# Kernel tuning notes

Hardware: AMD Instinct MI355X
Metric: run time of the kernel (lower is better)

The kernel has to match this reference:

```python
import jax, jax.numpy as jnp
import numpy as np

# anchor encoding indices: [x,y,z,log w,log l,log h,sin,cos,vx,vy,vz]
NUM_HEADS = 8
LN_EPS = 1e-5


def layer_norm(x, g, b):
    mu = jnp.mean(x, axis=-1, keepdims=True)
    var = jnp.var(x, axis=-1, keepdims=True)
    return (x - mu) * jax.lax.rsqrt(var + LN_EPS) * g + b


def align_anchors_to_frame(anchor, Tm):
    # anchor: (..., N, 11), Tm: (..., 4, 4)
    R = Tm[..., :3, :3]
    t = Tm[..., :3, 3]
    center = jnp.einsum('...ij,...nj->...ni', R, anchor[..., 0:3]) + t[..., None, :]
    size = anchor[..., 3:6]
    yaw = jnp.einsum('...ij,...nj->...ni', R[..., :2, :2], anchor[..., 6:8])
    vel = jnp.einsum('...ij,...nj->...ni', R, anchor[..., 8:11])
    return jnp.concatenate([center, size, yaw, vel], axis=-1)


def setup_inputs() -> dict:
    key = jax.random.key(0)
    ks = jax.random.split(key, 12)
    B, T, N, C, E, A = 2, 12, 1024, 256, 256, 11
    inp = {
        'seq_features': jax.random.normal(ks[0], (B, T, N, C), jnp.float32),
        'seq_anchors': jax.random.normal(ks[1], (B, T, N, A), jnp.float32),
        'T_ego_his2cur': jax.random.normal(ks[2], (B, T, 4, 4), jnp.float32),
        'Wf': jax.random.normal(ks[3], (E, C), jnp.float32) * (C ** -0.5),
        'bf': jnp.zeros((E,), jnp.float32),
        'Wa': jax.random.normal(ks[4], (E, A), jnp.float32) * (A ** -0.5),
        'ba': jnp.zeros((E,), jnp.float32),
        'Win': jax.random.normal(ks[5], (3 * E, E), jnp.float32) * (E ** -0.5),
        'bin_': jnp.zeros((3 * E,), jnp.float32),
        'gamma': jnp.ones((E,), jnp.float32),
        'beta': jnp.zeros((E,), jnp.float32),
    }
    return inp


def reference(seq_features, seq_anchors, T_ego_his2cur, Wf, bf, Wa, ba, Win, bin_, gamma, beta):
    B, T, N, C = seq_features.shape
    E = gamma.shape[0]
    H = NUM_HEADS
    D = E // H

    feat_cur = seq_features[:, 1:]    # (B,T-1,N,C)
    feat_prev = seq_features[:, :-1]
    anc_cur = seq_anchors[:, 1:]
    anc_prev = align_anchors_to_frame(seq_anchors[:, :-1], T_ego_his2cur[:, 1:])

    tok_cur = layer_norm(feat_cur @ Wf.T + bf + anc_cur @ Wa.T + ba, gamma, beta)
    tok_prev = layer_norm(feat_prev @ Wf.T + bf + anc_prev @ Wa.T + ba, gamma, beta)

    Wq, Wk = Win[:E], Win[E:2 * E]
    bq, bk = bin_[:E], bin_[E:2 * E]
    scale = np.float32(D) ** np.float32(-0.5)
    q = ((tok_cur @ Wq.T + bq) * scale).reshape(B, T - 1, N, H, D)
    k = (tok_prev @ Wk.T + bk).reshape(B, T - 1, N, H, D)

    scores = jnp.einsum('btnhd,btmhd->bthnm', q, k)  # (B,T-1,H,N,N)
    attn = jax.nn.softmax(scores, axis=-1).mean(axis=2)  # head-averaged weights

    eye = jnp.broadcast_to(jnp.eye(N, dtype=seq_features.dtype), (B, 1, N, N))
    return jnp.concatenate([eye, attn], axis=1)  # (B,T,N,N)
```

## Files before the change

kernel.cpp:

```cpp
#include <hip/hip_runtime.h>
#include <hip/hip_bf16.h>
#include <math.h>

#define LN_EPS 1e-5f

typedef short bf16x8 __attribute__((ext_vector_type(8)));
typedef float f32x4 __attribute__((ext_vector_type(4)));

__device__ inline short f2bf(float f) {
  union { float f; unsigned u; } v; v.f = f;
  unsigned r = v.u + 0x7FFFu + ((v.u >> 16) & 1u);
  return (short)(r >> 16);
}
__device__ inline float bf2f(unsigned short s) {
  union { unsigned u; float f; } v; v.u = ((unsigned)s) << 16;
  return v.f;
}
__device__ inline float fast_exp2(float x) {
#if __has_builtin(__builtin_amdgcn_exp2f)
  return __builtin_amdgcn_exp2f(x);
#else
  return __expf(x * 0.69314718056f);
#endif
}

__global__ __launch_bounds__(256) void convert_kernel(const float* __restrict__ Wf,
    const float* __restrict__ Win, short* __restrict__ Wfb, short* __restrict__ Wqkb)
{
  size_t i = ((size_t)blockIdx.x * 256 + threadIdx.x) * 8;
  const float* src;
  short* dst;
  if (i < 65536) { src = Wf + i; dst = Wfb + i; }
  else { src = Win + (i - 65536); dst = Wqkb + (i - 65536); }
  f32x4 x0 = *(const f32x4*)src;
  f32x4 x1 = *(const f32x4*)(src + 4);
  bf16x8 v;
  v[0] = f2bf(x0[0]); v[1] = f2bf(x0[1]); v[2] = f2bf(x0[2]); v[3] = f2bf(x0[3]);
  v[4] = f2bf(x1[0]); v[5] = f2bf(x1[1]); v[6] = f2bf(x1[2]); v[7] = f2bf(x1[3]);
  *(bf16x8*)dst = v;
}

__global__ __launch_bounds__(256, 2) void feat_ln(const float* __restrict__ Af,
    const short* __restrict__ Wb, const float* __restrict__ bfv,
    const float* __restrict__ anchors, const float* __restrict__ Tego,
    const float* __restrict__ Wa, const float* __restrict__ ba,
    const float* __restrict__ gamma, const float* __restrict__ beta,
    short* __restrict__ tok_cur, short* __restrict__ tok_prev)
{
  const int which = blockIdx.y;
  const int row0 = blockIdx.x * 64;
  const int s24 = row0 >> 10;
  const int b = s24 / 12, t = s24 - b * 12;
  if (which == 0 && t == 0) return;
  if (which == 1 && t == 11) return;

  __shared__ short ldb[256][40];
  __shared__ float ldWaT[11][256];
  __shared__ float aST[11][64];
  const int tid = threadIdx.x;
  const int wid = tid >> 6, lane = tid & 63;
  const int quad = lane >> 4, l15 = lane & 15;
  const int n0 = row0 & 1023;
  const int srow = tid >> 2, sseg = tid & 3;

  {
    float wv[11];
    #pragma unroll
    for (int jj = 0; jj < 11; ++jj) wv[jj] = Wa[(size_t)tid * 11 + jj];
    #pragma unroll
    for (int jj = 0; jj < 11; ++jj) ldWaT[jj][tid] = wv[jj];
  }
  if (tid < 64) {
    const float* ap = anchors + ((size_t)s24 * 1024 + n0 + tid) * 11;
    float a[11];
    #pragma unroll
    for (int j = 0; j < 11; ++j) a[j] = ap[j];
    if (which == 1) {
      const float* Tm = Tego + ((size_t)b * 12 + t + 1) * 16;
      float r00 = Tm[0], r01 = Tm[1], r02 = Tm[2],  t0 = Tm[3];
      float r10 = Tm[4], r11 = Tm[5], r12 = Tm[6],  t1 = Tm[7];
      float r20 = Tm[8], r21 = Tm[9], r22 = Tm[10], t2 = Tm[11];
      float a0 = a[0], a1 = a[1], a2 = a[2];
      float a6 = a[6], a7 = a[7], a8 = a[8], a9 = a[9], a10 = a[10];
      a[0] = r00 * a0 + r01 * a1 + r02 * a2 + t0;
      a[1] = r10 * a0 + r11 * a1 + r12 * a2 + t1;
      a[2] = r20 * a0 + r21 * a1 + r22 * a2 + t2;
      a[6] = r00 * a6 + r01 * a7;
      a[7] = r10 * a6 + r11 * a7;
      a[8] = r00 * a8 + r01 * a9 + r02 * a10;
      a[9] = r10 * a8 + r11 * a9 + r12 * a10;
      a[10] = r20 * a8 + r21 * a9 + r22 * a10;
    }
    #pragma unroll
    for (int j = 0; j < 11; ++j) aST[j][tid] = a[j];
  }

  f32x4 z = {0.f, 0.f, 0.f, 0.f};
  f32x4 acc[16];
  #pragma unroll
  for (int j = 0; j < 16; ++j) acc[j] = z;

  const float* arp = Af + (size_t)(row0 + wid * 16 + l15) * 256 + quad * 8;
  const short* wgp = Wb + (size_t)srow * 256 + sseg * 8;

  f32x4 xa0 = *(const f32x4*)(arp);
  f32x4 xa1 = *(const f32x4*)(arp + 4);

  #pragma unroll 1
  for (int ks = 0; ks < 8; ++ks) {
    const int kk = ks * 32;
    bf16x8 w0 = *(const bf16x8*)(wgp + kk);
    bf16x8 w1 = *(const bf16x8*)(wgp + 64 * 256 + kk);
    bf16x8 w2 = *(const bf16x8*)(wgp + 128 * 256 + kk);
    bf16x8 w3 = *(const bf16x8*)(wgp + 192 * 256 + kk);
    bf16x8 af;
    af[0] = f2bf(xa0[0]); af[1] = f2bf(xa0[1]); af[2] = f2bf(xa0[2]); af[3] = f2bf(xa0[3]);
    af[4] = f2bf(xa1[0]); af[5] = f2bf(xa1[1]); af[6] = f2bf(xa1[2]); af[7] = f2bf(xa1[3]);
    if (ks < 7) {
      xa0 = *(const f32x4*)(arp + kk + 32);
      xa1 = *(const f32x4*)(arp + kk + 36);
    }
    *(bf16x8*)&ldb[srow][sseg * 8]       = w0;
    *(bf16x8*)&ldb[srow + 64][sseg * 8]  = w1;
    *(bf16x8*)&ldb[srow + 128][sseg * 8] = w2;
    *(bf16x8*)&ldb[srow + 192][sseg * 8] = w3;
    __syncthreads();
    #pragma unroll
    for (int j = 0; j < 16; ++j) {
      bf16x8 bq = *(const bf16x8*)&ldb[j * 16 + l15][quad * 8];
      acc[j] = __builtin_amdgcn_mfma_f32_16x16x32_bf16(af, bq, acc[j], 0, 0, 0);
    }
    __syncthreads();
  }

  const int rbase = wid * 16 + quad * 4;
  #pragma unroll
  for (int jj = 0; jj < 11; ++jj) {
    f32x4 av = *(const f32x4*)&aST[jj][rbase];
    #pragma unroll
    for (int j = 0; j < 16; ++j) {
      float wv = ldWaT[jj][j * 16 + l15];
      #pragma unroll
      for (int r = 0; r < 4; ++r) acc[j][r] += wv * av[r];
    }
  }

  float s1[4] = {0.f, 0.f, 0.f, 0.f};
  float s2[4] = {0.f, 0.f, 0.f, 0.f};
  #pragma unroll
  for (int j = 0; j < 16; ++j) {
    const int col = j * 16 + l15;
    const float cb = bfv[col] + ba[col];
    #pragma unroll
    for (int r = 0; r < 4; ++r) {
      float v = acc[j][r] + cb;
      acc[j][r] = v;
      s1[r] += v; s2[r] += v * v;
    }
  }
  #pragma unroll
  for (int r = 0; r < 4; ++r) {
    #pragma unroll
    for (int off = 1; off < 16; off <<= 1) {
      s1[r] += __shfl_xor(s1[r], off);
      s2[r] += __shfl_xor(s2[r], off);
    }
  }
  float mean[4], rstd[4];
  #pragma unroll
  for (int r = 0; r < 4; ++r) {
    mean[r] = s1[r] * (1.0f / 256.0f);
    float var = s2[r] * (1.0f / 256.0f) - mean[r] * mean[r];
    rstd[r] = rsqrtf(var + LN_EPS);
  }

  short* dst = which ? tok_prev : tok_cur;
  const size_t tokbase = which ? (size_t)(b * 11 + t) * 1024
                               : (size_t)(b * 11 + t - 1) * 1024;
  #pragma unroll
  for (int j = 0; j < 16; ++j) {
    const int col = j * 16 + l15;
    const float g = gamma[col], be = beta[col];
    #pragma unroll
    for (int r = 0; r < 4; ++r) {
      const int n = n0 + wid * 16 + quad * 4 + r;
      dst[(tokbase + n) * 256 + col] = f2bf((acc[j][r] - mean[r]) * rstd[r] * g + be);
    }
  }
}

__global__ __launch_bounds__(256) void gemm_qk(const short* __restrict__ tokc,
    const short* __restrict__ tokp, const short* __restrict__ Wqkb,
    const float* __restrict__ binv, short* __restrict__ qb, short* __restrict__ kb)
{
  const int sel = blockIdx.z;
  const short* Ap = sel ? tokp : tokc;
  const short* W = Wqkb + (size_t)sel * 65536;
  const float* bias = binv + sel * 256;
  const float alpha = sel ? 1.0f : 0.17677669529663687f * 1.4426950408889634f;
  short* Out = sel ? kb : qb;

  __shared__ short lda[128][40];
  __shared__ short ldb[128][40];
  const int tid = threadIdx.x;
  const int bm = blockIdx.x * 128, bn = blockIdx.y * 128;
  const int wid = tid >> 6, lane = tid & 63;
  const int quad = lane >> 4, l15 = lane & 15;
  const int wm = (wid & 1) * 64, wn = (wid >> 1) * 64;
  const int srow = tid >> 2, sseg = tid & 3;

  f32x4 z = {0.f, 0.f, 0.f, 0.f};
  f32x4 acc[4][4];
  #pragma unroll
  for (int i = 0; i < 4; ++i)
    #pragma unroll
    for (int j = 0; j < 4; ++j) acc[i][j] = z;

  const short* a0 = Ap + (size_t)(bm + srow) * 256 + sseg * 8;
  const short* a1 = Ap + (size_t)(bm + srow + 64) * 256 + sseg * 8;
  const short* b0 = W + (size_t)(bn + srow) * 256 + sseg * 8;
  const short* b1 = W + (size_t)(bn + srow + 64) * 256 + sseg * 8;

  for (int kk = 0; kk < 256; kk += 32) {
    *(bf16x8*)&lda[srow][sseg * 8]      = *(const bf16x8*)(a0 + kk);
    *(bf16x8*)&lda[srow + 64][sseg * 8] = *(const bf16x8*)(a1 + kk);
    *(bf16x8*)&ldb[srow][sseg * 8]      = *(const bf16x8*)(b0 + kk);
    *(bf16x8*)&ldb[srow + 64][sseg * 8] = *(const bf16x8*)(b1 + kk);
    __syncthreads();
    bf16x8 af[4], bq[4];
    #pragma unroll
    for (int i = 0; i < 4; ++i) {
      af[i] = *(const bf16x8*)&lda[wm + i * 16 + l15][quad * 8];
      bq[i] = *(const bf16x8*)&ldb[wn + i * 16 + l15][quad * 8];
    }
    #pragma unroll
    for (int i = 0; i < 4; ++i)
      #pragma unroll
      for (int j = 0; j < 4; ++j)
        acc[i][j] = __builtin_amdgcn_mfma_f32_16x16x32_bf16(af[i], bq[j], acc[i][j], 0, 0, 0);
    __syncthreads();
  }

  #pragma unroll
  for (int i = 0; i < 4; ++i)
    #pragma unroll
    for (int j = 0; j < 4; ++j)
      #pragma unroll
      for (int r = 0; r < 4; ++r) {
        int grow = bm + wm + i * 16 + quad * 4 + r;
        int gcol = bn + wn + j * 16 + l15;
        float v = (acc[i][j][r] + bias[gcol]) * alpha;
        int btr = grow >> 10, nn = grow & 1023, h = gcol >> 5, d = gcol & 31;
        Out[(((size_t)btr * 8 + h) * 1024 + nn) * 32 + d] = f2bf(v);
      }
}

__global__ __launch_bounds__(256) void denom_kernel(const short* __restrict__ q,
  const short* __restrict__ k, float* __restrict__ dinv)
{
  __shared__ short kst[2][4096];
  const int tid = threadIdx.x, wid = tid >> 6, lane = tid & 63;
  const int quad = lane >> 4, l15 = lane & 15;
  const int h = blockIdx.y, bt = blockIdx.z;
  const int n0 = blockIdx.x * 128 + wid * 32;
  const size_t base = ((size_t)bt * 8 + h) * 32768;
  bf16x8 qf0 = *(const bf16x8*)(q + base + (size_t)(n0 + l15) * 32 + quad * 8);
  bf16x8 qf1 = *(const bf16x8*)(q + base + (size_t)(n0 + 16 + l15) * 32 + quad * 8);
  const short* ksA = k + base + (size_t)(wid * 16) * 32 + lane * 8;
  const short* ksB = k + base + (size_t)((wid + 4) * 16) * 32 + lane * 8;
  const int wswz = ((lane & 3) ^ ((lane >> 3) & 3)) * 8;
  const int rswz = (quad ^ ((l15 >> 1) & 3)) * 8;
  short* lwA = &kst[0][wid * 512 + (lane >> 2) * 32 + wswz];
  short* lwB = &kst[0][(wid + 4) * 512 + (lane >> 2) * 32 + wswz];

  f32x4 z = {0.f, 0.f, 0.f, 0.f};
  float s0 = 0.f, s1 = 0.f;

  bf16x8 stA = *(const bf16x8*)ksA;
  bf16x8 stB = *(const bf16x8*)ksB;
  *(bf16x8*)lwA = stA;
  *(bf16x8*)lwB = stB;
  __syncthreads();

  #pragma unroll 1
  for (int rd = 0; rd < 8; ++rd) {
    const int buf = rd & 1;
    if (rd < 7) {
      stA = *(const bf16x8*)(ksA + (size_t)(rd + 1) * 128 * 32);
      stB = *(const bf16x8*)(ksB + (size_t)(rd + 1) * 128 * 32);
    }
    #pragma unroll
    for (int s = 0; s < 8; ++s) {
      bf16x8 kf = *(const bf16x8*)&kst[buf][s * 512 + l15 * 32 + rswz];
      f32x4 c0 = __builtin_amdgcn_mfma_f32_16x16x32_bf16(kf, qf0, z, 0, 0, 0);
      f32x4 c1 = __builtin_amdgcn_mfma_f32_16x16x32_bf16(kf, qf1, z, 0, 0, 0);
      s0 += fast_exp2(c0[0]) + fast_exp2(c0[1]) + fast_exp2(c0[2]) + fast_exp2(c0[3]);
      s1 += fast_exp2(c1[0]) + fast_exp2(c1[1]) + fast_exp2(c1[2]) + fast_exp2(c1[3]);
    }
    if (rd < 7) {
      *(bf16x8*)(lwA + ((buf ^ 1) << 12)) = stA;
      *(bf16x8*)(lwB + ((buf ^ 1) << 12)) = stB;
    }
    __syncthreads();
  }
  s0 += __shfl_xor(s0, 16); s0 += __shfl_xor(s0, 32);
  s1 += __shfl_xor(s1, 16); s1 += __shfl_xor(s1, 32);
  if (quad == 0) {
    float* dp = dinv + ((size_t)bt * 8 + h) * 1024 + n0;
    dp[l15] = 1.f / s0;
    dp[16 + l15] = 1.f / s1;
  }
}

__global__ __launch_bounds__(256) void prob_kernel(const short* __restrict__ q,
  const short* __restrict__ k, const float* __restrict__ dinv, float* __restrict__ out)
{
  __shared__ short kst[2][4096];
  const int tid = threadIdx.x, wid = tid >> 6, lane = tid & 63;
  const int quad = lane >> 4, l15 = lane & 15;
  const int bt = blockIdx.z;
  const int n0 = blockIdx.x * 128 + wid * 32;
  const int mbase = blockIdx.y * 128;
  const int b = bt / 11, t = bt - b * 11;

  bf16x8 qf0[8], qf1[8];
  float invd0[8], invd1[8];
  #pragma unroll
  for (int h = 0; h < 8; ++h) {
    const size_t base = ((size_t)bt * 8 + h) * 32768;
    qf0[h] = *(const bf16x8*)(q + base + (size_t)(n0 + l15) * 32 + quad * 8);
    qf1[h] = *(const bf16x8*)(q + base + (size_t)(n0 + 16 + l15) * 32 + quad * 8);
    invd0[h] = dinv[((size_t)bt * 8 + h) * 1024 + n0 + l15] * 0.125f;
    invd1[h] = dinv[((size_t)bt * 8 + h) * 1024 + n0 + 16 + l15] * 0.125f;
  }
  const short* ksA = k + (((size_t)bt * 8 + wid    ) * 1024 + mbase) * 32 + lane * 8;
  const short* ksB = k + (((size_t)bt * 8 + wid + 4) * 1024 + mbase) * 32 + lane * 8;
  const int wswz = ((lane & 3) ^ ((lane >> 3) & 3)) * 8;
  const int rswz = (quad ^ ((l15 >> 1) & 3)) * 8;
  short* lwA = &kst[0][wid * 512 + (lane >> 2) * 32 + wswz];
  short* lwB = &kst[0][(wid + 4) * 512 + (lane >> 2) * 32 + wswz];

  float* ob0 = out + ((size_t)(b * 12 + t + 1) * 1024 + n0 + l15) * 1024
                   + mbase + quad * 4;
  float* ob1 = ob0 + (size_t)16 * 1024;
  f32x4 z = {0.f, 0.f, 0.f, 0.f};

  bf16x8 stA = *(const bf16x8*)ksA;
  bf16x8 stB = *(const bf16x8*)ksB;
  *(bf16x8*)lwA = stA;
  *(bf16x8*)lwB = stB;
  __syncthreads();

  #pragma unroll 1
  for (int mt = 0; mt < 8; ++mt) {
    const int buf = mt & 1;
    if (mt < 7) {
      stA = *(const bf16x8*)(ksA + (size_t)(mt + 1) * 16 * 32);
      stB = *(const bf16x8*)(ksB + (size_t)(mt + 1) * 16 * 32);
    }
    f32x4 P0 = z, P1 = z;
    #pragma unroll
    for (int h = 0; h < 8; ++h) {
      bf16x8 kf = *(const bf16x8*)&kst[buf][h * 512 + l15 * 32 + rswz];
      f32x4 c0 = __builtin_amdgcn_mfma_f32_16x16x32_bf16(kf, qf0[h], z, 0, 0, 0);
      f32x4 c1 = __builtin_amdgcn_mfma_f32_16x16x32_bf16(kf, qf1[h], z, 0, 0, 0);
      #pragma unroll
      for (int r = 0; r < 4; ++r) {
        P0[r] += fast_exp2(c0[r]) * invd0[h];
        P1[r] += fast_exp2(c1[r]) * invd1[h];
      }
    }
    *(f32x4*)(ob0 + mt * 16) = P0;
    *(f32x4*)(ob1 + mt * 16) = P1;
    if (mt < 7) {
      *(bf16x8*)(lwA + ((buf ^ 1) << 12)) = stA;
      *(bf16x8*)(lwB + ((buf ^ 1) << 12)) = stB;
    }
    __syncthreads();
  }
}

__global__ __launch_bounds__(256) void eye_kernel(float* __restrict__ out) {
  int gid = blockIdx.x * 256 + threadIdx.x;
  int b = gid >> 18, rem = gid & 262143;
  int n = rem >> 8, m4 = rem & 255;
  f32x4 v = {0.f, 0.f, 0.f, 0.f};
  int c = n - m4 * 4;
  if (c >= 0 && c < 4) v[c] = 1.0f;
  *(f32x4*)(out + (size_t)b * 12582912 + (size_t)n * 1024 + m4 * 4) = v;
}

extern "C" void kernel_launch(void* const* d_in, const int* in_sizes, int n_in,
                              void* d_out, int out_size, void* d_ws, size_t ws_size,
                              hipStream_t stream)
{
  const float* sf   = (const float*)d_in[0];
  const float* sa   = (const float*)d_in[1];
  const float* te   = (const float*)d_in[2];
  const float* Wf   = (const float*)d_in[3];
  const float* bfv  = (const float*)d_in[4];
  const float* Wa   = (const float*)d_in[5];
  const float* ba   = (const float*)d_in[6];
  const float* Win  = (const float*)d_in[7];
  const float* binv = (const float*)d_in[8];
  const float* gam  = (const float*)d_in[9];
  const float* bet  = (const float*)d_in[10];
  float* out = (float*)d_out;

  char* w = (char*)d_ws;
  short* tok_cur  = (short*)w;  w += 11534336;
  short* tok_prev = (short*)w;  w += 11534336;
  short* qb       = (short*)w;  w += 11534336;
  short* kb       = (short*)w;  w += 11534336;
  float* dinv     = (float*)w;  w += 720896;
  short* Wfb      = (short*)w;  w += 131072;
  short* Wqkb     = (short*)w;  w += 262144;

  convert_kernel<<<dim3(96), 256, 0, stream>>>(Wf, Win, Wfb, Wqkb);
  feat_ln<<<dim3(384, 2), 256, 0, stream>>>(sf, Wfb, bfv, sa, te, Wa, ba, gam, bet,
                                            tok_cur, tok_prev);
  gemm_qk<<<dim3(176, 2, 2), 256, 0, stream>>>(tok_cur, tok_prev, Wqkb, binv, qb, kb);
  denom_kernel<<<dim3(8, 8, 22), 256, 0, stream>>>(qb, kb, dinv);
  prob_kernel<<<dim3(8, 8, 22), 256, 0, stream>>>(qb, kb, dinv, out);
  eye_kernel<<<dim3(2048), 256, 0, stream>>>(out);
}
```

Baseline: 247.8 us.

## Share feature GEMM between cur/prev tokens and vectorize QK epilogue stores

feat_ln now runs once per 64-row feature block and reuses the feature projection for both the current-frame and previous-frame token outputs, applying separate anchor terms and LayerNorm for each. This halves the large fp32 feature reads and MFMA work in the token stage, at the cost of more registers from the second accumulator set and half as many blocks. Separately, gemm_qk swaps the MFMA operands so each lane holds four consecutive output columns, letting it write 4 bf16 values with a single short4 store and a vector bias load instead of scattered scalar stores.

New measurement: 245.2 us. Within noise of the previous version (-1.1%).

```diff
diff --git a/kernel.cpp b/kernel.cpp
--- a/kernel.cpp
+++ b/kernel.cpp
@@ -47,22 +47,22 @@
     const float* __restrict__ gamma, const float* __restrict__ beta,
     short* __restrict__ tok_cur, short* __restrict__ tok_prev)
 {
-  const int which = blockIdx.y;
   const int row0 = blockIdx.x * 64;
   const int s24 = row0 >> 10;
   const int b = s24 / 12, t = s24 - b * 12;
-  if (which == 0 && t == 0) return;
-  if (which == 1 && t == 11) return;
 
   __shared__ short ldb[256][40];
   __shared__ float ldWaT[11][256];
-  __shared__ float aST[11][64];
+  __shared__ float aSTc[11][64];
+  __shared__ float aSTp[11][64];
+  __shared__ float cbS[256];
   const int tid = threadIdx.x;
   const int wid = tid >> 6, lane = tid & 63;
   const int quad = lane >> 4, l15 = lane & 15;
   const int n0 = row0 & 1023;
   const int srow = tid >> 2, sseg = tid & 3;
 
+  cbS[tid] = bfv[tid] + ba[tid];
   {
     float wv[11];
     #pragma unroll
@@ -75,24 +75,26 @@
     float a[11];
     #pragma unroll
     for (int j = 0; j < 11; ++j) a[j] = ap[j];
-    if (which == 1) {
+    #pragma unroll
+    for (int j = 0; j < 11; ++j) aSTc[j][tid] = a[j];
+    if (t <= 10) {
       const float* Tm = Tego + ((size_t)b * 12 + t + 1) * 16;
       float r00 = Tm[0], r01 = Tm[1], r02 = Tm[2],  t0 = Tm[3];
       float r10 = Tm[4], r11 = Tm[5], r12 = Tm[6],  t1 = Tm[7];
       float r20 = Tm[8], r21 = Tm[9], r22 = Tm[10], t2 = Tm[11];
-      float a0 = a[0], a1 = a[1], a2 = a[2];
-      float a6 = a[6], a7 = a[7], a8 = a[8], a9 = a[9], a10 = a[10];
-      a[0] = r00 * a0 + r01 * a1 + r02 * a2 + t0;
-      a[1] = r10 * a0 + r11 * a1 + r12 * a2 + t1;
-      a[2] = r20 * a0 + r21 * a1 + r22 * a2 + t2;
-      a[6] = r00 * a6 + r01 * a7;
-      a[7] = r10 * a6 + r11 * a7;
-      a[8] = r00 * a8 + r01 * a9 + r02 * a10;
-      a[9] = r10 * a8 + r11 * a9 + r12 * a10;
-      a[10] = r20 * a8 + r21 * a9 + r22 * a10;
-    }
-    #pragma unroll
-    for (int j = 0; j < 11; ++j) aST[j][tid] = a[j];
+      float p0 = r00 * a[0] + r01 * a[1] + r02 * a[2] + t0;
+      float p1 = r10 * a[0] + r11 * a[1] + r12 * a[2] + t1;
+      float p2 = r20 * a[0] + r21 * a[1] + r22 * a[2] + t2;
+      float p6 = r00 * a[6] + r01 * a[7];
+      float p7 = r10 * a[6] + r11 * a[7];
+      float p8 = r00 * a[8] + r01 * a[9] + r02 * a[10];
+      float p9 = r10 * a[8] + r11 * a[9] + r12 * a[10];
+      float p10 = r20 * a[8] + r21 * a[9] + r22 * a[10];
+      aSTp[0][tid] = p0;  aSTp[1][tid] = p1;  aSTp[2][tid] = p2;
+      aSTp[3][tid] = a[3]; aSTp[4][tid] = a[4]; aSTp[5][tid] = a[5];
+      aSTp[6][tid] = p6;  aSTp[7][tid] = p7;
+      aSTp[8][tid] = p8;  aSTp[9][tid] = p9;  aSTp[10][tid] = p10;
+    }
   }
 
   f32x4 z = {0.f, 0.f, 0.f, 0.f};
@@ -134,59 +136,61 @@
   }
 
   const int rbase = wid * 16 + quad * 4;
-  #pragma unroll
-  for (int jj = 0; jj < 11; ++jj) {
-    f32x4 av = *(const f32x4*)&aST[jj][rbase];
+  auto emit = [&](const float (*aST)[64], short* dst, size_t tokbase) {
+    f32x4 d[16];
+    #pragma unroll
+    for (int j = 0; j < 16; ++j) d[j] = z;
+    #pragma unroll
+    for (int jj = 0; jj < 11; ++jj) {
+      f32x4 av = *(const f32x4*)&aST[jj][rbase];
+      #pragma unroll
+      for (int j = 0; j < 16; ++j) {
+        float wv = ldWaT[jj][j * 16 + l15];
+        #pragma unroll
+        for (int r = 0; r < 4; ++r) d[j][r] += wv * av[r];
+      }
+    }
+    float s1[4] = {0.f, 0.f, 0.f, 0.f};
+    float s2[4] = {0.f, 0.f, 0.f, 0.f};
     #pragma unroll
     for (int j = 0; j < 16; ++j) {
-      float wv = ldWaT[jj][j * 16 + l15];
-      #pragma unroll
-      for (int r = 0; r < 4; ++r) acc[j][r] += wv * av[r];
-    }
-  }
-
-  float s1[4] = {0.f, 0.f, 0.f, 0.f};
-  float s2[4] = {0.f, 0.f, 0.f, 0.f};
-  #pragma unroll
-  for (int j = 0; j < 16; ++j) {
-    const int col = j * 16 + l15;
-    const float cb = bfv[col] + ba[col];
+      const float cb = cbS[j * 16 + l15];
+      #pragma unroll
+      for (int r = 0; r < 4; ++r) {
+        float v = acc[j][r] + cb + d[j][r];
+        d[j][r] = v;
+        s1[r] += v; s2[r] += v * v;
+      }
+    }
     #pragma unroll
     for (int r = 0; r < 4; ++r) {
-      float v = acc[j][r] + cb;
-      acc[j][r] = v;
-      s1[r] += v; s2[r] += v * v;
-    }
-  }
-  #pragma unroll
-  for (int r = 0; r < 4; ++r) {
-    #pragma unroll
-    for (int off = 1; off < 16; off <<= 1) {
-      s1[r] += __shfl_xor(s1[r], off);
-      s2[r] += __shfl_xor(s2[r], off);
-    }
-  }
-  float mean[4], rstd[4];
-  #pragma unroll
-  for (int r = 0; r < 4; ++r) {
-    mean[r] = s1[r] * (1.0f / 256.0f);
-    float var = s2[r] * (1.0f / 256.0f) - mean[r] * mean[r];
-    rstd[r] = rsqrtf(var + LN_EPS);
-  }
-
-  short* dst = which ? tok_prev : tok_cur;
-  const size_t tokbase = which ? (size_t)(b * 11 + t) * 1024
-                               : (size_t)(b * 11 + t - 1) * 1024;
-  #pragma unroll
-  for (int j = 0; j < 16; ++j) {
-    const int col = j * 16 + l15;
-    const float g = gamma[col], be = beta[col];
+      #pragma unroll
+      for (int off = 1; off < 16; off <<= 1) {
+        s1[r] += __shfl_xor(s1[r], off);
+        s2[r] += __shfl_xor(s2[r], off);
+      }
+    }
+    float mean[4], rstd[4];
     #pragma unroll
     for (int r = 0; r < 4; ++r) {
-      const int n = n0 + wid * 16 + quad * 4 + r;
-      dst[(tokbase + n) * 256 + col] = f2bf((acc[j][r] - mean[r]) * rstd[r] * g + be);
-    }
-  }
+      mean[r] = s1[r] * (1.0f / 256.0f);
+      float var = s2[r] * (1.0f / 256.0f) - mean[r] * mean[r];
+      rstd[r] = rsqrtf(var + LN_EPS);
+    }
+    #pragma unroll
+    for (int j = 0; j < 16; ++j) {
+      const int col = j * 16 + l15;
+      const float g = gamma[col], be = beta[col];
+      #pragma unroll
+      for (int r = 0; r < 4; ++r) {
+        const int n = n0 + wid * 16 + quad * 4 + r;
+        dst[(tokbase + n) * 256 + col] = f2bf((d[j][r] - mean[r]) * rstd[r] * g + be);
+      }
+    }
+  };
+
+  if (t >= 1)  emit(aSTc, tok_cur,  (size_t)(b * 11 + t - 1) * 1024);
+  if (t <= 10) emit(aSTp, tok_prev, (size_t)(b * 11 + t) * 1024);
 }
 
 __global__ __launch_bounds__(256) void gemm_qk(const short* __restrict__ tokc,
@@ -237,22 +241,28 @@
     for (int i = 0; i < 4; ++i)
       #pragma unroll
       for (int j = 0; j < 4; ++j)
-        acc[i][j] = __builtin_amdgcn_mfma_f32_16x16x32_bf16(af[i], bq[j], acc[i][j], 0, 0, 0);
+        acc[i][j] = __builtin_amdgcn_mfma_f32_16x16x32_bf16(bq[j], af[i], acc[i][j], 0, 0, 0);
     __syncthreads();
   }
 
   #pragma unroll
-  for (int i = 0; i < 4; ++i)
-    #pragma unroll
-    for (int j = 0; j < 4; ++j)
-      #pragma unroll
-      for (int r = 0; r < 4; ++r) {
-        int grow = bm + wm + i * 16 + quad * 4 + r;
-        int gcol = bn + wn + j * 16 + l15;
-        float v = (acc[i][j][r] + bias[gcol]) * alpha;
-        int btr = grow >> 10, nn = grow & 1023, h = gcol >> 5, d = gcol & 31;
-        Out[(((size_t)btr * 8 + h) * 1024 + nn) * 32 + d] = f2bf(v);
-      }
+  for (int i = 0; i < 4; ++i) {
+    const int grow = bm + wm + i * 16 + l15;
+    const int btr = grow >> 10, nn = grow & 1023;
+    #pragma unroll
+    for (int j = 0; j < 4; ++j) {
+      const int gcol0 = bn + wn + j * 16;
+      const int h = gcol0 >> 5;
+      const int d0 = (gcol0 & 31) + quad * 4;
+      f32x4 bv = *(const f32x4*)(bias + gcol0 + quad * 4);
+      short4 o;
+      o.x = f2bf((acc[i][j][0] + bv[0]) * alpha);
+      o.y = f2bf((acc[i][j][1] + bv[1]) * alpha);
+      o.z = f2bf((acc[i][j][2] + bv[2]) * alpha);
+      o.w = f2bf((acc[i][j][3] + bv[3]) * alpha);
+      *(short4*)(Out + (((size_t)btr * 8 + h) * 1024 + nn) * 32 + d0) = o;
+    }
+  }
 }
 
 __global__ __launch_bounds__(256) void denom_kernel(const short* __restrict__ q,
@@ -417,8 +427,8 @@
   short* Wqkb     = (short*)w;  w += 262144;
 
   convert_kernel<<<dim3(96), 256, 0, stream>>>(Wf, Win, Wfb, Wqkb);
-  feat_ln<<<dim3(384, 2), 256, 0, stream>>>(sf, Wfb, bfv, sa, te, Wa, ba, gam, bet,
-                                            tok_cur, tok_prev);
+  feat_ln<<<dim3(384), 256, 0, stream>>>(sf, Wfb, bfv, sa, te, Wa, ba, gam, bet,
+                                         tok_cur, tok_prev);
   gemm_qk<<<dim3(176, 2, 2), 256, 0, stream>>>(tok_cur, tok_prev, Wqkb, binv, qb, kb);
   denom_kernel<<<dim3(8, 8, 22), 256, 0, stream>>>(qb, kb, dinv);
   prob_kernel<<<dim3(8, 8, 22), 256, 0, stream>>>(qb, kb, dinv, out);
```

## Fuse feature projection, layer norm and Q/K projection into one kernel

Applied to the files above, without the earlier changes.

Merges the feat_ln and gemm_qk kernels. Each block now computes the shared feature GEMM once for a 64-row tile and produces both the cur and prev token variants from it, since only the anchor term differs. It then layer-normalizes both, stages them in LDS as bf16, and projects them to Q and K directly with weights read from global memory. This removes the tok_cur/tok_prev round trip through global memory, one kernel launch, and the duplicated feature GEMM. In exchange it uses more LDS and registers per block, and the Q/K projection runs with only 384 blocks and unstaged weight loads.

Measured after the change: 269.4 us. 8.7% more time.

```diff
diff --git a/kernel.cpp b/kernel.cpp
--- a/kernel.cpp
+++ b/kernel.cpp
@@ -40,29 +40,35 @@
   *(bf16x8*)dst = v;
 }
 
-__global__ __launch_bounds__(256, 2) void feat_ln(const float* __restrict__ Af,
+__global__ __launch_bounds__(256, 2) void feat_qk(const float* __restrict__ Af,
     const short* __restrict__ Wb, const float* __restrict__ bfv,
     const float* __restrict__ anchors, const float* __restrict__ Tego,
     const float* __restrict__ Wa, const float* __restrict__ ba,
     const float* __restrict__ gamma, const float* __restrict__ beta,
-    short* __restrict__ tok_cur, short* __restrict__ tok_prev)
+    const short* __restrict__ Wqkb, const float* __restrict__ binv,
+    short* __restrict__ qb, short* __restrict__ kb)
 {
-  const int which = blockIdx.y;
   const int row0 = blockIdx.x * 64;
   const int s24 = row0 >> 10;
   const int b = s24 / 12, t = s24 - b * 12;
-  if (which == 0 && t == 0) return;
-  if (which == 1 && t == 11) return;
-
-  __shared__ short ldb[256][40];
-  __shared__ float ldWaT[11][256];
-  __shared__ float aST[11][64];
+  const bool do_cur = (t >= 1), do_prev = (t <= 10);
+
+  __shared__ __attribute__((aligned(16))) char smem[67584];
+  short (*ldb)[40]    = (short(*)[40])(smem);
+  float (*ldWaT)[256] = (float(*)[256])(smem + 20480);
+  float (*aSTc)[64]   = (float(*)[64])(smem + 31744);
+  float (*aSTp)[64]   = (float(*)[64])(smem + 34560);
+  float* cbS          = (float*)(smem + 37376);
+  short (*Acur)[264]  = (short(*)[264])(smem);
+  short (*Aprev)[264] = (short(*)[264])(smem + 33792);
+
   const int tid = threadIdx.x;
   const int wid = tid >> 6, lane = tid & 63;
   const int quad = lane >> 4, l15 = lane & 15;
   const int n0 = row0 & 1023;
   const int srow = tid >> 2, sseg = tid & 3;
 
+  cbS[tid] = bfv[tid] + ba[tid];
   {
     float wv[11];
     #pragma unroll
@@ -75,24 +81,23 @@
     float a[11];
     #pragma unroll
     for (int j = 0; j < 11; ++j) a[j] = ap[j];
-    if (which == 1) {
+    #pragma unroll
+    for (int j = 0; j < 11; ++j) aSTc[j][tid] = a[j];
+    if (do_prev) {
       const float* Tm = Tego + ((size_t)b * 12 + t + 1) * 16;
       float r00 = Tm[0], r01 = Tm[1], r02 = Tm[2],  t0 = Tm[3];
       float r10 = Tm[4], r11 = Tm[5], r12 = Tm[6],  t1 = Tm[7];
       float r20 = Tm[8], r21 = Tm[9], r22 = Tm[10], t2 = Tm[11];
-      float a0 = a[0], a1 = a[1], a2 = a[2];
-      float a6 = a[6], a7 = a[7], a8 = a[8], a9 = a[9], a10 = a[10];
-      a[0] = r00 * a0 + r01 * a1 + r02 * a2 + t0;
-      a[1] = r10 * a0 + r11 * a1 + r12 * a2 + t1;
-      a[2] = r20 * a0 + r21 * a1 + r22 * a2 + t2;
-      a[6] = r00 * a6 + r01 * a7;
-      a[7] = r10 * a6 + r11 * a7;
-      a[8] = r00 * a8 + r01 * a9 + r02 * a10;
-      a[9] = r10 * a8 + r11 * a9 + r12 * a10;
-      a[10] = r20 * a8 + r21 * a9 + r22 * a10;
-    }
-    #pragma unroll
-    for (int j = 0; j < 11; ++j) aST[j][tid] = a[j];
+      aSTp[0][tid] = r00 * a[0] + r01 * a[1] + r02 * a[2] + t0;
+      aSTp[1][tid] = r10 * a[0] + r11 * a[1] + r12 * a[2] + t1;
+      aSTp[2][tid] = r20 * a[0] + r21 * a[1] + r22 * a[2] + t2;
+      aSTp[3][tid] = a[3]; aSTp[4][tid] = a[4]; aSTp[5][tid] = a[5];
+      aSTp[6][tid] = r00 * a[6] + r01 * a[7];
+      aSTp[7][tid] = r10 * a[6] + r11 * a[7];
+      aSTp[8][tid] = r00 * a[8] + r01 * a[9] + r02 * a[10];
+      aSTp[9][tid] = r10 * a[8] + r11 * a[9] + r12 * a[10];
+      aSTp[10][tid] = r20 * a[8] + r21 * a[9] + r22 * a[10];
+    }
   }
 
   f32x4 z = {0.f, 0.f, 0.f, 0.f};
@@ -102,7 +107,6 @@
 
   const float* arp = Af + (size_t)(row0 + wid * 16 + l15) * 256 + quad * 8;
   const short* wgp = Wb + (size_t)srow * 256 + sseg * 8;
-
   f32x4 xa0 = *(const f32x4*)(arp);
   f32x4 xa1 = *(const f32x4*)(arp + 4);
 
@@ -134,125 +138,123 @@
   }
 
   const int rbase = wid * 16 + quad * 4;
+  f32x4 vcur[16], vprev[16];
+
+  #pragma unroll
+  for (int j = 0; j < 16; ++j) { vcur[j] = z; vprev[j] = z; }
   #pragma unroll
   for (int jj = 0; jj < 11; ++jj) {
-    f32x4 av = *(const f32x4*)&aST[jj][rbase];
+    f32x4 avc = *(const f32x4*)&aSTc[jj][rbase];
+    f32x4 avp = *(const f32x4*)&aSTp[jj][rbase];
     #pragma unroll
     for (int j = 0; j < 16; ++j) {
       float wv = ldWaT[jj][j * 16 + l15];
       #pragma unroll
-      for (int r = 0; r < 4; ++r) acc[j][r] += wv * av[r];
-    }
-  }
-
-  float s1[4] = {0.f, 0.f, 0.f, 0.f};
-  float s2[4] = {0.f, 0.f, 0.f, 0.f};
+      for (int r = 0; r < 4; ++r) {
+        vcur[j][r] += wv * avc[r];
+        vprev[j][r] += wv * avp[r];
+      }
+    }
+  }
+  float s1c[4] = {0,0,0,0}, s2c[4] = {0,0,0,0};
+  float s1p[4] = {0,0,0,0}, s2p[4] = {0,0,0,0};
   #pragma unroll
   for (int j = 0; j < 16; ++j) {
-    const int col = j * 16 + l15;
-    const float cb = bfv[col] + ba[col];
+    const float cb = cbS[j * 16 + l15];
     #pragma unroll
     for (int r = 0; r < 4; ++r) {
-      float v = acc[j][r] + cb;
-      acc[j][r] = v;
-      s1[r] += v; s2[r] += v * v;
+      float vc = acc[j][r] + cb + vcur[j][r];
+      float vp = acc[j][r] + cb + vprev[j][r];
+      vcur[j][r] = vc; vprev[j][r] = vp;
+      s1c[r] += vc; s2c[r] += vc * vc;
+      s1p[r] += vp; s2p[r] += vp * vp;
     }
   }
   #pragma unroll
   for (int r = 0; r < 4; ++r) {
     #pragma unroll
     for (int off = 1; off < 16; off <<= 1) {
-      s1[r] += __shfl_xor(s1[r], off);
-      s2[r] += __shfl_xor(s2[r], off);
-    }
-  }
-  float mean[4], rstd[4];
+      s1c[r] += __shfl_xor(s1c[r], off); s2c[r] += __shfl_xor(s2c[r], off);
+      s1p[r] += __shfl_xor(s1p[r], off); s2p[r] += __shfl_xor(s2p[r], off);
+    }
+  }
+  float mc[4], rc[4], mp[4], rp[4];
   #pragma unroll
   for (int r = 0; r < 4; ++r) {
-    mean[r] = s1[r] * (1.0f / 256.0f);
-    float var = s2[r] * (1.0f / 256.0f) - mean[r] * mean[r];
-    rstd[r] = rsqrtf(var + LN_EPS);
-  }
-
-  short* dst = which ? tok_prev : tok_cur;
-  const size_t tokbase = which ? (size_t)(b * 11 + t) * 1024
-                               : (size_t)(b * 11 + t - 1) * 1024;
+    mc[r] = s1c[r] * (1.0f / 256.0f);
+    rc[r] = rsqrtf(s2c[r] * (1.0f / 256.0f) - mc[r] * mc[r] + LN_EPS);
+    mp[r] = s1p[r] * (1.0f / 256.0f);
+    rp[r] = rsqrtf(s2p[r] * (1.0f / 256.0f) - mp[r] * mp[r] + LN_EPS);
+  }
   #pragma unroll
   for (int j = 0; j < 16; ++j) {
     const int col = j * 16 + l15;
     const float g = gamma[col], be = beta[col];
     #pragma unroll
     for (int r = 0; r < 4; ++r) {
-      const int n = n0 + wid * 16 + quad * 4 + r;
-      dst[(tokbase + n) * 256 + col] = f2bf((acc[j][r] - mean[r]) * rstd[r] * g + be);
-    }
-  }
-}
-
-__global__ __launch_bounds__(256) void gemm_qk(const short* __restrict__ tokc,
-    const short* __restrict__ tokp, const short* __restrict__ Wqkb,
-    const float* __restrict__ binv, short* __restrict__ qb, short* __restrict__ kb)
-{
-  const int sel = blockIdx.z;
-  const short* Ap = sel ? tokp : tokc;
-  const short* W = Wqkb + (size_t)sel * 65536;
-  const float* bias = binv + sel * 256;
-  const float alpha = sel ? 1.0f : 0.17677669529663687f * 1.4426950408889634f;
-  short* Out = sel ? kb : qb;
-
-  __shared__ short lda[128][40];
-  __shared__ short ldb[128][40];
-  const int tid = threadIdx.x;
-  const int bm = blockIdx.x * 128, bn = blockIdx.y * 128;
-  const int wid = tid >> 6, lane = tid & 63;
-  const int quad = lane >> 4, l15 = lane & 15;
-  const int wm = (wid & 1) * 64, wn = (wid >> 1) * 64;
-  const int srow = tid >> 2, sseg = tid & 3;
-
-  f32x4 z = {0.f, 0.f, 0.f, 0.f};
-  f32x4 acc[4][4];
-  #pragma unroll
-  for (int i = 0; i < 4; ++i)
-    #pragma unroll
-    for (int j = 0; j < 4; ++j) acc[i][j] = z;
-
-  const short* a0 = Ap + (size_t)(bm + srow) * 256 + sseg * 8;
-  const short* a1 = Ap + (size_t)(bm + srow + 64) * 256 + sseg * 8;
-  const short* b0 = W + (size_t)(bn + srow) * 256 + sseg * 8;
-  const short* b1 = W + (size_t)(bn + srow + 64) * 256 + sseg * 8;
-
-  for (int kk = 0; kk < 256; kk += 32) {
-    *(bf16x8*)&lda[srow][sseg * 8]      = *(const bf16x8*)(a0 + kk);
-    *(bf16x8*)&lda[srow + 64][sseg * 8] = *(const bf16x8*)(a1 + kk);
-    *(bf16x8*)&ldb[srow][sseg * 8]      = *(const bf16x8*)(b0 + kk);
-    *(bf16x8*)&ldb[srow + 64][sseg * 8] = *(const bf16x8*)(b1 + kk);
-    __syncthreads();
-    bf16x8 af[4], bq[4];
+      vcur[j][r]  = (vcur[j][r]  - mc[r]) * rc[r] * g + be;
+      vprev[j][r] = (vprev[j][r] - mp[r]) * rp[r] * g + be;
+    }
+  }
+
+  __syncthreads();
+  #pragma unroll
+  for (int j = 0; j < 16; ++j)
+    #pragma unroll
+    for (int r = 0; r < 4; ++r) {
+      Acur[rbase + r][j * 16 + l15]  = f2bf(vcur[j][r]);
+      Aprev[rbase + r][j * 16 + l15] = f2bf(vprev[j][r]);
+    }
+  __syncthreads();
+
+  const int wn = wid * 64;
+  auto proj = [&](const short (*At)[264], const short* W, const float* bias,
+                  float alpha, short* Out, int btr) {
+    f32x4 a2[4][4];
+    #pragma unroll
+    for (int i = 0; i < 4; ++i)
+      #pragma unroll
+      for (int j = 0; j < 4; ++j) a2[i][j] = z;
+    const short* wrp = W + (size_t)(wn + l15) * 256 + quad * 8;
+    #pragma unroll 1
+    for (int kk = 0; kk < 256; kk += 32) {
+      bf16x8 af[4], bq[4];
+      #pragma unroll
+      for (int i = 0; i < 4; ++i)
+        af[i] = *(const bf16x8*)&At[i * 16 + l15][kk + quad * 8];
+      #pragma unroll
+      for (int j = 0; j < 4; ++j)
+        bq[j] = *(const bf16x8*)(wrp + (size_t)j * 16 * 256 + kk);
+      #pragma unroll
+      for (int i = 0; i < 4; ++i)
+        #pragma unroll
+        for (int j = 0; j < 4; ++j)
+          a2[i][j] = __builtin_amdgcn_mfma_f32_16x16x32_bf16(bq[j], af[i], a2[i][j], 0, 0, 0);
+    }
     #pragma unroll
     for (int i = 0; i < 4; ++i) {
-      af[i] = *(const bf16x8*)&lda[wm + i * 16 + l15][quad * 8];
-      bq[i] = *(const bf16x8*)&ldb[wn + i * 16 + l15][quad * 8];
-    }
-    #pragma unroll
-    for (int i = 0; i < 4; ++i)
-      #pragma unroll
-      for (int j = 0; j < 4; ++j)
-        acc[i][j] = __builtin_amdgcn_mfma_f32_16x16x32_bf16(af[i], bq[j], acc[i][j], 0, 0, 0);
-    __syncthreads();
-  }
-
-  #pragma unroll
-  for (int i = 0; i < 4; ++i)
-    #pragma unroll
-    for (int j = 0; j < 4; ++j)
-      #pragma unroll
-      for (int r = 0; r < 4; ++r) {
-        int grow = bm + wm + i * 16 + quad * 4 + r;
-        int gcol = bn + wn + j * 16 + l15;
-        float v = (acc[i][j][r] + bias[gcol]) * alpha;
-        int btr = grow >> 10, nn = grow & 1023, h = gcol >> 5, d = gcol & 31;
-        Out[(((size_t)btr * 8 + h) * 1024 + nn) * 32 + d] = f2bf(v);
+      const int n = n0 + i * 16 + l15;
+      #pragma unroll
+      for (int j = 0; j < 4; ++j) {
+        const int col0 = wn + j * 16;
+        const int h = col0 >> 5;
+        const int d0 = (col0 & 31) + quad * 4;
+        f32x4 bv = *(const f32x4*)(bias + col0 + quad * 4);
+        short4 o;
+        o.x = f2bf((a2[i][j][0] + bv[0]) * alpha);
+        o.y = f2bf((a2[i][j][1] + bv[1]) * alpha);
+        o.z = f2bf((a2[i][j][2] + bv[2]) * alpha);
+        o.w = f2bf((a2[i][j][3] + bv[3]) * alpha);
+        *(short4*)(Out + (((size_t)btr * 8 + h) * 1024 + n) * 32 + d0) = o;
       }
+    }
+  };
+
+  if (do_cur)
+    proj(Acur, Wqkb, binv, 0.17677669529663687f * 1.4426950408889634f,
+         qb, b * 11 + t - 1);
+  if (do_prev)
+    proj(Aprev, Wqkb + 65536, binv + 256, 1.0f, kb, b * 11 + t);
 }
 
 __global__ __launch_bounds__(256) void denom_kernel(const short* __restrict__ q,
@@ -408,8 +410,6 @@
   float* out = (float*)d_out;
 
   char* w = (char*)d_ws;
-  short* tok_cur  = (short*)w;  w += 11534336;
-  short* tok_prev = (short*)w;  w += 11534336;
   short* qb       = (short*)w;  w += 11534336;
   short* kb       = (short*)w;  w += 11534336;
   float* dinv     = (float*)w;  w += 720896;
@@ -417,9 +417,8 @@
   short* Wqkb     = (short*)w;  w += 262144;
 
   convert_kernel<<<dim3(96), 256, 0, stream>>>(Wf, Win, Wfb, Wqkb);
-  feat_ln<<<dim3(384, 2), 256, 0, stream>>>(sf, Wfb, bfv, sa, te, Wa, ba, gam, bet,
-                                            tok_cur, tok_prev);
-  gemm_qk<<<dim3(176, 2, 2), 256, 0, stream>>>(tok_cur, tok_prev, Wqkb, binv, qb, kb);
+  feat_qk<<<dim3(384), 256, 0, stream>>>(sf, Wfb, bfv, sa, te, Wa, ba, gam, bet,
+                                         Wqkb, binv, qb, kb);
   denom_kernel<<<dim3(8, 8, 22), 256, 0, stream>>>(qb, kb, dinv);
   prob_kernel<<<dim3(8, 8, 22), 256, 0, stream>>>(qb, kb, dinv, out);
   eye_kernel<<<dim3(2048), 256, 0, stream>>>(out);
```
